# Optimization experiments

Measured on AMD Instinct MI355X. Metric: run time of the kernel, lower is better.

Reference implementation:

```python
import jax, jax.numpy as jnp
import numpy as np

S, B, E, H, V = 512, 256, 256, 256, 50000


def setup_inputs() -> dict:
    key = jax.random.key(0)
    ks = jax.random.split(key, 16)
    sc = 0.05
    return {
        "s1": jax.random.randint(ks[0], (S, B), 0, V, dtype=jnp.int32),
        "s2": jax.random.randint(ks[1], (S, B), 0, V, dtype=jnp.int32),
        "emb": jax.random.normal(ks[2], (V, E), jnp.float32) * sc,
        "W_ih": jax.random.normal(ks[3], (4 * H, E), jnp.float32) * sc,
        "W_hh": jax.random.normal(ks[4], (4 * H, H), jnp.float32) * sc,
        "b_ih": jax.random.normal(ks[5], (4 * H,), jnp.float32) * sc,
        "b_hh": jax.random.normal(ks[6], (4 * H,), jnp.float32) * sc,
        "h0_1": jax.random.normal(ks[7], (B, H), jnp.float32),
        "c0_1": jax.random.normal(ks[8], (B, H), jnp.float32),
        "h0_2": jax.random.normal(ks[9], (B, H), jnp.float32),
        "c0_2": jax.random.normal(ks[10], (B, H), jnp.float32),
        "W1": jax.random.normal(ks[11], (H, 2 * H), jnp.float32) * sc,
        "b1": jax.random.normal(ks[12], (H,), jnp.float32) * sc,
        "W2": jax.random.normal(ks[13], (2, H), jnp.float32) * sc,
        "b2": jax.random.normal(ks[14], (2,), jnp.float32) * sc,
    }


def _lstm(tokens, emb, W_ih, W_hh, b_ih, b_hh, h0, c0):
    # tokens: [S, B] int; returns final hidden h: [B, H]
    x = emb[tokens]  # [S, B, E]
    b = b_ih + b_hh

    def step(carry, xt):
        h, c = carry
        gates = xt @ W_ih.T + h @ W_hh.T + b  # [B, 4H]
        i, f, g, o = jnp.split(gates, 4, axis=-1)  # PyTorch gate order
        i = jax.nn.sigmoid(i)
        f = jax.nn.sigmoid(f)
        g = jnp.tanh(g)
        o = jax.nn.sigmoid(o)
        c = f * c + i * g
        h = o * jnp.tanh(c)
        return (h, c), None

    (h, c), _ = jax.lax.scan(step, (h0, c0), x)
    return h


def reference(s1, s2, emb, W_ih, W_hh, b_ih, b_hh, h0_1, c0_1, h0_2, c0_2, W1, b1, W2, b2):
    v1 = _lstm(s1, emb, W_ih, W_hh, b_ih, b_hh, h0_1, c0_1)  # [B, H]
    v2 = _lstm(s2, emb, W_ih, W_hh, b_ih, b_hh, h0_2, c0_2)  # [B, H]
    feat = jnp.concatenate([v1, v2], axis=-1)  # [B, 2H]
    hid = feat @ W1.T + b1  # no activation, per original Sequential
    out = hid @ W2.T + b2  # [B, 2]
    return out
```

## Files before the change

### kernel.cpp

```cpp
#include <hip/hip_runtime.h>
#include <hip/hip_bf16.h>

#define SS 512
#define BB 256
#define EE 256
#define HH 256
#define VV 50000
#define NCH 512
#define VR 16

#define NGRP 32
#define NSLC 8

#define CTRL_CNT 0
#define CTRL_START 32
#define CTRL_UNSAFE 33
#define CTRL_CLAIMG 34
#define CTRL_CLAIMX 40
#define CTRL_FLAGS 64
#define CTRL_N (64 + NGRP * NSLC * 16)

__device__ __forceinline__ float sigf(float x) { return 1.f / (1.f + __expf(-x)); }
__device__ __forceinline__ float tanhf_fast(float x) { return 1.f - 2.f / (__expf(2.f * x) + 1.f); }

__global__ void pack_w4(const float* __restrict__ W, float4* __restrict__ Wp, int K) {
    int idx = blockIdx.x * blockDim.x + threadIdx.x;
    if (idx >= K * HH) return;
    int k = idx >> 8, t = idx & 255;
    Wp[idx] = make_float4(W[(0 * HH + t) * K + k], W[(1 * HH + t) * K + k],
                          W[(2 * HH + t) * K + k], W[(3 * HH + t) * K + k]);
}

__global__ void pack_b(const float* __restrict__ bi, const float* __restrict__ bh,
                       float4* __restrict__ bp) {
    int t = threadIdx.x;
    bp[t] = make_float4(bi[0 * HH + t] + bh[0 * HH + t], bi[1 * HH + t] + bh[1 * HH + t],
                        bi[2 * HH + t] + bh[2 * HH + t], bi[3 * HH + t] + bh[3 * HH + t]);
}

__global__ void transpose_w1(const float* __restrict__ W1, float* __restrict__ W1T) {
    int idx = blockIdx.x * blockDim.x + threadIdx.x;
    if (idx >= 2 * HH * HH) return;
    int k = idx >> 8, j = idx & 255;
    W1T[idx] = W1[j * (2 * HH) + k];
}

__global__ void zero_ctrl(int* __restrict__ p) {
    int i = blockIdx.x * blockDim.x + threadIdx.x;
    if (i < CTRL_N) p[i] = 0;
}

__global__ __launch_bounds__(256) void embw_kernel(const float* __restrict__ emb,
                                                   const float4* __restrict__ Wip,
                                                   const float4* __restrict__ bp,
                                                   float4* __restrict__ embWp) {
    __shared__ float se[VR][EE];
    int t = threadIdx.x;
    int v0 = blockIdx.x * VR;
    for (int r = 0; r < VR; ++r) se[r][t] = emb[(size_t)(v0 + r) * EE + t];
    __syncthreads();
    float4 bb = bp[t];
    float4 acc[VR];
#pragma unroll
    for (int r = 0; r < VR; ++r) acc[r] = bb;
#pragma unroll 2
    for (int k = 0; k < EE; ++k) {
        float4 w = Wip[k * HH + t];
#pragma unroll
        for (int r = 0; r < VR; ++r) {
            float x = se[r][k];
            acc[r].x += w.x * x; acc[r].y += w.y * x;
            acc[r].z += w.z * x; acc[r].w += w.w * x;
        }
    }
    for (int r = 0; r < VR; ++r) embWp[(size_t)(v0 + r) * HH + t] = acc[r];
}

__global__ __launch_bounds__(256, 1) void lstm_coop(
    const int* __restrict__ s1, const int* __restrict__ s2,
    const float4* __restrict__ Whp, const float4* __restrict__ embWp,
    const float* __restrict__ h0_1, const float* __restrict__ c0_1,
    const float* __restrict__ h0_2, const float* __restrict__ c0_2,
    float* __restrict__ feat, float* __restrict__ hbuf, int* __restrict__ ctrl) {
    __shared__ float4 w4s[256 * 32];
    __shared__ float4 hls4[256 * 4];
    __shared__ int shi[4];

    const int t = threadIdx.x;
    const int j = t & 31, ks = (t >> 5) & 1, mg = t >> 6;

    if (t == 0) {
        int my_xcd = (int)__builtin_amdgcn_s_getreg(63508) & 7;
        int slot = atomicAdd(&ctrl[CTRL_CLAIMX + my_xcd], 1);
        int wall = atomicAdd(&ctrl[CTRL_CLAIMG], 1);
        if (slot >= 32)
            __hip_atomic_fetch_or(&ctrl[CTRL_UNSAFE], 1, __ATOMIC_RELAXED,
                                  __HIP_MEMORY_SCOPE_AGENT);
        __hip_atomic_fetch_add(&ctrl[CTRL_START], 1, __ATOMIC_RELEASE,
                               __HIP_MEMORY_SCOPE_AGENT);
        long it = 0;
        while (__hip_atomic_load(&ctrl[CTRL_START], __ATOMIC_ACQUIRE,
                                 __HIP_MEMORY_SCOPE_AGENT) < NGRP * NSLC) {
            if (++it >= 3000000L) break;
            __builtin_amdgcn_s_sleep(2);
        }
        int uns = __hip_atomic_load(&ctrl[CTRL_UNSAFE], __ATOMIC_ACQUIRE,
                                    __HIP_MEMORY_SCOPE_AGENT);
        if (uns) { shi[0] = wall >> 3; shi[1] = wall & 7; }
        else     { shi[0] = my_xcd * 4 + (slot >> 3); shi[1] = slot & 7; }
        shi[2] = uns;
    }
    __syncthreads();
    const int gid = shi[0];
    const int u = shi[1];
    const bool safe = (shi[2] == 0);
    const int u32j = u * 32 + j;

    for (int idx = t; idx < 256 * 32; idx += 256)
        w4s[idx] = Whp[(idx >> 5) * HH + u * 32 + (idx & 31)];

    const bool tw2 = gid >= 16;
    const float* h0x = tw2 ? h0_2 : h0_1;
    const float* c0x = tw2 ? c0_2 : c0_1;
    const int* tp = tw2 ? s2 : s1;
    const int gb = (gid & 15) * 16;

    float* hptr = (float*)hls4;
#pragma unroll
    for (int q = 0; q < 16; ++q) {
        int e = t + q * 256;
        hptr[e] = h0x[(gb + (e & 15)) * HH + (e >> 4)];
    }
    float c[4];
#pragma unroll
    for (int i = 0; i < 4; ++i) c[i] = c0x[(gb + mg * 4 + i) * HH + u32j];
    __syncthreads();

    const int bq0 = gb + mg * 4 + 2 * ks;
    float4 pfv[2]; int tnx[2];
    {
        int tk0 = tp[0 * BB + bq0], tk1 = tp[0 * BB + bq0 + 1];
        pfv[0] = embWp[(size_t)tk0 * HH + u32j];
        pfv[1] = embWp[(size_t)tk1 * HH + u32j];
        tnx[0] = tp[1 * BB + bq0];
        tnx[1] = tp[1 * BB + bq0 + 1];
    }

    const float4* wp = w4s + ks * 128 * 32 + j;
    const float4* hp = hls4 + ks * 128 * 4 + mg;
    volatile int* fl = (volatile int*)(ctrl + CTRL_FLAGS + gid * NSLC * 16);
    int dead = 0;

    for (int s = 0; s < SS; ++s) {
        float4 pf2[2]; int t2[2];
        pf2[0] = embWp[(size_t)tnx[0] * HH + u32j];
        pf2[1] = embWp[(size_t)tnx[1] * HH + u32j];
        int sn = (s + 2 < SS) ? s + 2 : SS - 1;
        t2[0] = tp[sn * BB + bq0];
        t2[1] = tp[sn * BB + bq0 + 1];

        float4 a0 = {0, 0, 0, 0}, a1 = {0, 0, 0, 0}, a2 = {0, 0, 0, 0}, a3 = {0, 0, 0, 0};
#pragma unroll 4
        for (int kk = 0; kk < 128; ++kk) {
            float4 w = wp[kk * 32];
            float4 h4 = hp[kk * 4];
            a0.x += w.x * h4.x; a0.y += w.y * h4.x; a0.z += w.z * h4.x; a0.w += w.w * h4.x;
            a1.x += w.x * h4.y; a1.y += w.y * h4.y; a1.z += w.z * h4.y; a1.w += w.w * h4.y;
            a2.x += w.x * h4.z; a2.y += w.y * h4.z; a2.z += w.z * h4.z; a2.w += w.w * h4.z;
            a3.x += w.x * h4.w; a3.y += w.y * h4.w; a3.z += w.z * h4.w; a3.w += w.w * h4.w;
        }
        if (ks == 0) {
            a0.x += pfv[0].x; a0.y += pfv[0].y; a0.z += pfv[0].z; a0.w += pfv[0].w;
            a1.x += pfv[1].x; a1.y += pfv[1].y; a1.z += pfv[1].z; a1.w += pfv[1].w;
        } else {
            a2.x += pfv[0].x; a2.y += pfv[0].y; a2.z += pfv[0].z; a2.w += pfv[0].w;
            a3.x += pfv[1].x; a3.y += pfv[1].y; a3.z += pfv[1].z; a3.w += pfv[1].w;
        }
        a0.x += __shfl_xor(a0.x, 32); a0.y += __shfl_xor(a0.y, 32);
        a0.z += __shfl_xor(a0.z, 32); a0.w += __shfl_xor(a0.w, 32);
        a1.x += __shfl_xor(a1.x, 32); a1.y += __shfl_xor(a1.y, 32);
        a1.z += __shfl_xor(a1.z, 32); a1.w += __shfl_xor(a1.w, 32);
        a2.x += __shfl_xor(a2.x, 32); a2.y += __shfl_xor(a2.y, 32);
        a2.z += __shfl_xor(a2.z, 32); a2.w += __shfl_xor(a2.w, 32);
        a3.x += __shfl_xor(a3.x, 32); a3.y += __shfl_xor(a3.y, 32);
        a3.z += __shfl_xor(a3.z, 32); a3.w += __shfl_xor(a3.w, 32);

        float hn[4];
        {
            float ig, fg, gg, og;
            ig = sigf(a0.x); fg = sigf(a0.y); gg = tanhf_fast(a0.z); og = sigf(a0.w);
            c[0] = fg * c[0] + ig * gg; hn[0] = og * tanhf_fast(c[0]);
            ig = sigf(a1.x); fg = sigf(a1.y); gg = tanhf_fast(a1.z); og = sigf(a1.w);
            c[1] = fg * c[1] + ig * gg; hn[1] = og * tanhf_fast(c[1]);
            ig = sigf(a2.x); fg = sigf(a2.y); gg = tanhf_fast(a2.z); og = sigf(a2.w);
            c[2] = fg * c[2] + ig * gg; hn[2] = og * tanhf_fast(c[2]);
            ig = sigf(a3.x); fg = sigf(a3.y); gg = tanhf_fast(a3.z); og = sigf(a3.w);
            c[3] = fg * c[3] + ig * gg; hn[3] = og * tanhf_fast(c[3]);
        }
        float* hx = hbuf + ((s + 1) & 1) * (NGRP * 16 * HH) + gid * (16 * HH);
        if (ks == 0) {
            *((float4*)(hx + u32j * 16 + mg * 4)) =
                make_float4(hn[0], hn[1], hn[2], hn[3]);
        }
        __syncthreads();
        if (safe) {
            if (t == 0) {
                fl[u * 16] = s + 1;
                if (!dead) {
                    long it = 0;
                    for (;;) {
                        int ok = 1;
#pragma unroll
                        for (int x = 0; x < NSLC; ++x) ok &= (fl[x * 16] >= s + 1);
                        if (ok) break;
                        if (++it >= 400000L) { dead = 1; break; }
                    }
                }
            }
        } else {
            __threadfence();
            if (t == 0) {
                atomicAdd(&ctrl[CTRL_CNT + gid], 1);
                int tgt = NSLC * (s + 1);
                if (!dead) {
                    long it = 0;
                    while (__hip_atomic_load(&ctrl[CTRL_CNT + gid], __ATOMIC_RELAXED,
                                             __HIP_MEMORY_SCOPE_AGENT) < tgt) {
                        if (++it >= 4000000L) { dead = 1; break; }
                        __builtin_amdgcn_s_sleep(2);
                    }
                }
            }
        }
        __syncthreads();
        if (!safe) __threadfence();
        const volatile float* hsrc = (const volatile float*)hx;
#pragma unroll
        for (int q = 0; q < 16; ++q) {
            int e = t + q * 256;
            hptr[e] = hsrc[e];
        }
        __syncthreads();
        pfv[0] = pf2[0]; pfv[1] = pf2[1];
        tnx[0] = t2[0]; tnx[1] = t2[1];
    }

    if (u == 0) {
#pragma unroll
        for (int q = 0; q < 16; ++q) {
            int e = t + q * 256;
            feat[(size_t)(gid * 16 + (e & 15)) * HH + (e >> 4)] = hptr[e];
        }
    }
}

#define NBF 4
__global__ __launch_bounds__(256, 1) void lstm_stream(
    const int* __restrict__ s1, const int* __restrict__ s2, const float* __restrict__ emb,
    const float4* __restrict__ Whp, const float4* __restrict__ Wip,
    const float4* __restrict__ bp,
    const float* __restrict__ h0_1, const float* __restrict__ c0_1,
    const float* __restrict__ h0_2, const float* __restrict__ c0_2,
    float* __restrict__ feat) {
    __shared__ float hs[NBF][HH];
    __shared__ float xs[NBF][EE];
    int t = threadIdx.x;
    int ch0 = blockIdx.x * NBF;
    float c[NBF];
    int bat[NBF];
    const int* toks[NBF];
#pragma unroll
    for (int nb = 0; nb < NBF; ++nb) {
        int ch = ch0 + nb;
        bool t2 = ch >= BB;
        int b = t2 ? ch - BB : ch;
        bat[nb] = b;
        toks[nb] = t2 ? s2 : s1;
        hs[nb][t] = (t2 ? h0_2 : h0_1)[b * HH + t];
        c[nb] = (t2 ? c0_2 : c0_1)[b * HH + t];
    }
    __syncthreads();
    for (int s = 0; s < SS; ++s) {
        float4 acc[NBF];
        float4 bb = bp[t];
#pragma unroll
        for (int nb = 0; nb < NBF; ++nb) {
            int tok = toks[nb][s * BB + bat[nb]];
            xs[nb][t] = emb[(size_t)tok * EE + t];
            acc[nb] = bb;
        }
        __syncthreads();
#pragma unroll 4
        for (int k = 0; k < EE; ++k) {
            float4 w = Wip[k * HH + t];
#pragma unroll
            for (int nb = 0; nb < NBF; ++nb) {
                float x = xs[nb][k];
                acc[nb].x += w.x * x; acc[nb].y += w.y * x;
                acc[nb].z += w.z * x; acc[nb].w += w.w * x;
            }
        }
#pragma unroll 8
        for (int k = 0; k < HH; ++k) {
            float4 w = Whp[k * HH + t];
#pragma unroll
            for (int nb = 0; nb < NBF; ++nb) {
                float hk = hs[nb][k];
                acc[nb].x += w.x * hk; acc[nb].y += w.y * hk;
                acc[nb].z += w.z * hk; acc[nb].w += w.w * hk;
            }
        }
        float hnew[NBF];
#pragma unroll
        for (int nb = 0; nb < NBF; ++nb) {
            float ig = sigf(acc[nb].x), fg = sigf(acc[nb].y);
            float gg = tanhf_fast(acc[nb].z), og = sigf(acc[nb].w);
            c[nb] = fg * c[nb] + ig * gg;
            hnew[nb] = og * tanhf_fast(c[nb]);
        }
        __syncthreads();
#pragma unroll
        for (int nb = 0; nb < NBF; ++nb) hs[nb][t] = hnew[nb];
        __syncthreads();
    }
#pragma unroll
    for (int nb = 0; nb < NBF; ++nb) feat[(size_t)(ch0 + nb) * HH + t] = hs[nb][t];
}

__global__ __launch_bounds__(256) void head_kernel(const float* __restrict__ feat,
                                                   const float* __restrict__ W1T,
                                                   const float* __restrict__ b1,
                                                   const float* __restrict__ W2,
                                                   const float* __restrict__ b2,
                                                   float* __restrict__ out) {
    __shared__ float f[2 * HH];
    __shared__ float r0[256], r1[256];
    int j = threadIdx.x;
    int b = blockIdx.x;
    f[j] = feat[(size_t)b * HH + j];
    f[HH + j] = feat[(size_t)(BB + b) * HH + j];
    __syncthreads();
    float acc = b1[j];
#pragma unroll 4
    for (int k = 0; k < 2 * HH; ++k) acc += f[k] * W1T[k * HH + j];
    r0[j] = acc * W2[0 * HH + j];
    r1[j] = acc * W2[1 * HH + j];
    __syncthreads();
    for (int st = 128; st > 0; st >>= 1) {
        if (j < st) { r0[j] += r0[j + st]; r1[j] += r1[j + st]; }
        __syncthreads();
    }
    if (j == 0) {
        out[b * 2 + 0] = r0[0] + b2[0];
        out[b * 2 + 1] = r1[0] + b2[1];
    }
}

extern "C" void kernel_launch(void* const* d_in, const int* in_sizes, int n_in,
                              void* d_out, int out_size, void* d_ws, size_t ws_size,
                              hipStream_t stream) {
    const int* s1 = (const int*)d_in[0];
    const int* s2 = (const int*)d_in[1];
    const float* emb = (const float*)d_in[2];
    const float* W_ih = (const float*)d_in[3];
    const float* W_hh = (const float*)d_in[4];
    const float* b_ih = (const float*)d_in[5];
    const float* b_hh = (const float*)d_in[6];
    const float* h0_1 = (const float*)d_in[7];
    const float* c0_1 = (const float*)d_in[8];
    const float* h0_2 = (const float*)d_in[9];
    const float* c0_2 = (const float*)d_in[10];
    const float* W1 = (const float*)d_in[11];
    const float* b1 = (const float*)d_in[12];
    const float* W2 = (const float*)d_in[13];
    const float* b2 = (const float*)d_in[14];
    float* out = (float*)d_out;

    char* ws = (char*)d_ws;
    size_t off = 0;
    auto alloc = [&](size_t bytes) {
        void* p = ws + off;
        off += (bytes + 255) & ~(size_t)255;
        return p;
    };
    float4* Whp = (float4*)alloc((size_t)HH * HH * sizeof(float4));
    float4* Wip = (float4*)alloc((size_t)EE * HH * sizeof(float4));
    float4* bp = (float4*)alloc(HH * sizeof(float4));
    float* W1T = (float*)alloc((size_t)2 * HH * HH * sizeof(float));
    float* feat = (float*)alloc((size_t)NCH * HH * sizeof(float));
    float* hbuf = (float*)alloc((size_t)2 * NGRP * 16 * HH * sizeof(float));
    int* ctrl = (int*)alloc(CTRL_N * sizeof(int));
    size_t embw_bytes = (size_t)VV * HH * sizeof(float4);
    bool pre = (ws_size >= off + embw_bytes);
    float4* embWp = pre ? (float4*)alloc(embw_bytes) : nullptr;

    pack_w4<<<(HH * HH + 255) / 256, 256, 0, stream>>>(W_ih, Wip, EE);
    pack_w4<<<(HH * HH + 255) / 256, 256, 0, stream>>>(W_hh, Whp, HH);
    pack_b<<<1, 256, 0, stream>>>(b_ih, b_hh, bp);
    transpose_w1<<<(2 * HH * HH + 255) / 256, 256, 0, stream>>>(W1, W1T);

    if (pre) {
        zero_ctrl<<<(CTRL_N + 255) / 256, 256, 0, stream>>>(ctrl);
        embw_kernel<<<VV / VR, 256, 0, stream>>>(emb, Wip, bp, embWp);
        lstm_coop<<<NGRP * NSLC, 256, 0, stream>>>(s1, s2, Whp, embWp,
                                                   h0_1, c0_1, h0_2, c0_2,
                                                   feat, hbuf, ctrl);
    } else {
        lstm_stream<<<NCH / NBF, 256, 0, stream>>>(s1, s2, emb, Whp, Wip, bp,
                                                   h0_1, c0_1, h0_2, c0_2, feat);
    }
    head_kernel<<<BB, 256, 0, stream>>>(feat, W1T, b1, W2, b2, out);
}
```

Measured before the change: 5.476 ms.

## Keep recurrent weights in registers and split K across lanes with shuffle reduction

The recurrent weight slice now lives in 32 float4 registers per thread instead of shared memory. Each thread handles one output column over a 32-wide K chunk for all 16 batch rows, and a three-level butterfly shuffle reduction combines the eight K chunks. The hidden-state exchange buffer is also laid out in padded 20-float blocks to avoid LDS bank conflicts. This removes the per-step weight reads from shared memory, but raises register pressure (128 VGPRs for weights plus 64 accumulators) and adds shuffle work.

```diff
diff --git a/kernel.cpp b/kernel.cpp
--- a/kernel.cpp
+++ b/kernel.cpp
@@ -11,6 +11,7 @@
 
 #define NGRP 32
 #define NSLC 8
+#define HWRD (256 * 20)
 
 #define CTRL_CNT 0
 #define CTRL_START 32
@@ -82,12 +83,12 @@
     const float* __restrict__ h0_1, const float* __restrict__ c0_1,
     const float* __restrict__ h0_2, const float* __restrict__ c0_2,
     float* __restrict__ feat, float* __restrict__ hbuf, int* __restrict__ ctrl) {
-    __shared__ float4 w4s[256 * 32];
-    __shared__ float4 hls4[256 * 4];
+    __shared__ float hls[16384 + HWRD];
     __shared__ int shi[4];
 
     const int t = threadIdx.x;
-    const int j = t & 31, ks = (t >> 5) & 1, mg = t >> 6;
+    const int w = t >> 6, l = t & 63;
+    const int kq = l >> 3, jl = l & 7;
 
     if (t == 0) {
         int my_xcd = (int)__builtin_amdgcn_s_getreg(63508) & 7;
@@ -114,10 +115,12 @@
     const int gid = shi[0];
     const int u = shi[1];
     const bool safe = (shi[2] == 0);
-    const int u32j = u * 32 + j;
-
-    for (int idx = t; idx < 256 * 32; idx += 256)
-        w4s[idx] = Whp[(idx >> 5) * HH + u * 32 + (idx & 31)];
+    const int gu = u * 32 + w * 8 + jl;
+
+    float4 wreg[32];
+#pragma unroll
+    for (int kk = 0; kk < 32; ++kk)
+        wreg[kk] = Whp[(kq * 32 + kk) * HH + gu];
 
     const bool tw2 = gid >= 16;
     const float* h0x = tw2 ? h0_2 : h0_1;
@@ -125,83 +128,106 @@
     const int* tp = tw2 ? s2 : s1;
     const int gb = (gid & 15) * 16;
 
-    float* hptr = (float*)hls4;
-#pragma unroll
-    for (int q = 0; q < 16; ++q) {
-        int e = t + q * 256;
-        hptr[e] = h0x[(gb + (e & 15)) * HH + (e >> 4)];
-    }
-    float c[4];
-#pragma unroll
-    for (int i = 0; i < 4; ++i) c[i] = c0x[(gb + mg * 4 + i) * HH + u32j];
-    __syncthreads();
-
-    const int bq0 = gb + mg * 4 + 2 * ks;
+    for (int e = t; e < HWRD; e += 256) {
+        int blk = e / 20, cc = e % 20;
+        int k = (blk & 7) * 32 + (blk >> 3);
+        hls[e] = (cc < 16) ? h0x[(gb + cc) * HH + k] : 0.f;
+    }
+    float cst[2];
+    cst[0] = c0x[(gb + 2 * kq + 0) * HH + gu];
+    cst[1] = c0x[(gb + 2 * kq + 1) * HH + gu];
+    __syncthreads();
+
+    const int bq0 = gb + 2 * kq;
     float4 pfv[2]; int tnx[2];
-    {
-        int tk0 = tp[0 * BB + bq0], tk1 = tp[0 * BB + bq0 + 1];
-        pfv[0] = embWp[(size_t)tk0 * HH + u32j];
-        pfv[1] = embWp[(size_t)tk1 * HH + u32j];
-        tnx[0] = tp[1 * BB + bq0];
-        tnx[1] = tp[1 * BB + bq0 + 1];
-    }
-
-    const float4* wp = w4s + ks * 128 * 32 + j;
-    const float4* hp = hls4 + ks * 128 * 4 + mg;
+    pfv[0] = embWp[(size_t)tp[bq0] * HH + gu];
+    pfv[1] = embWp[(size_t)tp[bq0 + 1] * HH + gu];
+    tnx[0] = tp[BB + bq0];
+    tnx[1] = tp[BB + bq0 + 1];
+
+    const float4* hl4 = (const float4*)hls;
     volatile int* fl = (volatile int*)(ctrl + CTRL_FLAGS + gid * NSLC * 16);
+    const int b0 = kq & 1, b1 = (kq >> 1) & 1, b2 = kq >> 2;
+    const int blkd = ((gu & 31) * 8 + (gu >> 5)) * 20 + 2 * kq;
     int dead = 0;
 
     for (int s = 0; s < SS; ++s) {
         float4 pf2[2]; int t2[2];
-        pf2[0] = embWp[(size_t)tnx[0] * HH + u32j];
-        pf2[1] = embWp[(size_t)tnx[1] * HH + u32j];
+        pf2[0] = embWp[(size_t)tnx[0] * HH + gu];
+        pf2[1] = embWp[(size_t)tnx[1] * HH + gu];
         int sn = (s + 2 < SS) ? s + 2 : SS - 1;
         t2[0] = tp[sn * BB + bq0];
         t2[1] = tp[sn * BB + bq0 + 1];
 
-        float4 a0 = {0, 0, 0, 0}, a1 = {0, 0, 0, 0}, a2 = {0, 0, 0, 0}, a3 = {0, 0, 0, 0};
-#pragma unroll 4
-        for (int kk = 0; kk < 128; ++kk) {
-            float4 w = wp[kk * 32];
-            float4 h4 = hp[kk * 4];
-            a0.x += w.x * h4.x; a0.y += w.y * h4.x; a0.z += w.z * h4.x; a0.w += w.w * h4.x;
-            a1.x += w.x * h4.y; a1.y += w.y * h4.y; a1.z += w.z * h4.y; a1.w += w.w * h4.y;
-            a2.x += w.x * h4.z; a2.y += w.y * h4.z; a2.z += w.z * h4.z; a2.w += w.w * h4.z;
-            a3.x += w.x * h4.w; a3.y += w.y * h4.w; a3.z += w.z * h4.w; a3.w += w.w * h4.w;
-        }
-        if (ks == 0) {
-            a0.x += pfv[0].x; a0.y += pfv[0].y; a0.z += pfv[0].z; a0.w += pfv[0].w;
-            a1.x += pfv[1].x; a1.y += pfv[1].y; a1.z += pfv[1].z; a1.w += pfv[1].w;
-        } else {
-            a2.x += pfv[0].x; a2.y += pfv[0].y; a2.z += pfv[0].z; a2.w += pfv[0].w;
-            a3.x += pfv[1].x; a3.y += pfv[1].y; a3.z += pfv[1].z; a3.w += pfv[1].w;
-        }
-        a0.x += __shfl_xor(a0.x, 32); a0.y += __shfl_xor(a0.y, 32);
-        a0.z += __shfl_xor(a0.z, 32); a0.w += __shfl_xor(a0.w, 32);
-        a1.x += __shfl_xor(a1.x, 32); a1.y += __shfl_xor(a1.y, 32);
-        a1.z += __shfl_xor(a1.z, 32); a1.w += __shfl_xor(a1.w, 32);
-        a2.x += __shfl_xor(a2.x, 32); a2.y += __shfl_xor(a2.y, 32);
-        a2.z += __shfl_xor(a2.z, 32); a2.w += __shfl_xor(a2.w, 32);
-        a3.x += __shfl_xor(a3.x, 32); a3.y += __shfl_xor(a3.y, 32);
-        a3.z += __shfl_xor(a3.z, 32); a3.w += __shfl_xor(a3.w, 32);
-
-        float hn[4];
+        float4 acc[16];
+#pragma unroll
+        for (int c = 0; c < 16; ++c) acc[c] = make_float4(0.f, 0.f, 0.f, 0.f);
+#pragma unroll
+        for (int kk = 0; kk < 32; ++kk) {
+            const float4 wv = wreg[kk];
+            const int base = (kk * 8 + kq) * 5;
+            const float4 hv0 = hl4[base + 0], hv1 = hl4[base + 1];
+            const float4 hv2 = hl4[base + 2], hv3 = hl4[base + 3];
+#define FMA4(C, HV) acc[C].x += wv.x * HV; acc[C].y += wv.y * HV; \
+                    acc[C].z += wv.z * HV; acc[C].w += wv.w * HV;
+            FMA4(0, hv0.x) FMA4(1, hv0.y) FMA4(2, hv0.z) FMA4(3, hv0.w)
+            FMA4(4, hv1.x) FMA4(5, hv1.y) FMA4(6, hv1.z) FMA4(7, hv1.w)
+            FMA4(8, hv2.x) FMA4(9, hv2.y) FMA4(10, hv2.z) FMA4(11, hv2.w)
+            FMA4(12, hv3.x) FMA4(13, hv3.y) FMA4(14, hv3.z) FMA4(15, hv3.w)
+#undef FMA4
+        }
+
+        float4 s1v[8];
         {
-            float ig, fg, gg, og;
-            ig = sigf(a0.x); fg = sigf(a0.y); gg = tanhf_fast(a0.z); og = sigf(a0.w);
-            c[0] = fg * c[0] + ig * gg; hn[0] = og * tanhf_fast(c[0]);
-            ig = sigf(a1.x); fg = sigf(a1.y); gg = tanhf_fast(a1.z); og = sigf(a1.w);
-            c[1] = fg * c[1] + ig * gg; hn[1] = og * tanhf_fast(c[1]);
-            ig = sigf(a2.x); fg = sigf(a2.y); gg = tanhf_fast(a2.z); og = sigf(a2.w);
-            c[2] = fg * c[2] + ig * gg; hn[2] = og * tanhf_fast(c[2]);
-            ig = sigf(a3.x); fg = sigf(a3.y); gg = tanhf_fast(a3.z); og = sigf(a3.w);
-            c[3] = fg * c[3] + ig * gg; hn[3] = og * tanhf_fast(c[3]);
-        }
-        float* hx = hbuf + ((s + 1) & 1) * (NGRP * 16 * HH) + gid * (16 * HH);
-        if (ks == 0) {
-            *((float4*)(hx + u32j * 16 + mg * 4)) =
-                make_float4(hn[0], hn[1], hn[2], hn[3]);
-        }
+#pragma unroll
+            for (int i = 0; i < 8; ++i) {
+                constexpr int LO[8] = {0, 1, 4, 5, 8, 9, 12, 13};
+                float4 xs = b0 ? acc[LO[i]] : acc[LO[i] + 2];
+                float4 kp = b0 ? acc[LO[i] + 2] : acc[LO[i]];
+                s1v[i].x = kp.x + __shfl_xor(xs.x, 8);
+                s1v[i].y = kp.y + __shfl_xor(xs.y, 8);
+                s1v[i].z = kp.z + __shfl_xor(xs.z, 8);
+                s1v[i].w = kp.w + __shfl_xor(xs.w, 8);
+            }
+        }
+        float4 s2v[4];
+        {
+#pragma unroll
+            for (int i = 0; i < 4; ++i) {
+                constexpr int A2[4] = {0, 1, 4, 5};
+                float4 xs = b1 ? s1v[A2[i]] : s1v[A2[i] ^ 2];
+                float4 kp = b1 ? s1v[A2[i] ^ 2] : s1v[A2[i]];
+                s2v[i].x = kp.x + __shfl_xor(xs.x, 16);
+                s2v[i].y = kp.y + __shfl_xor(xs.y, 16);
+                s2v[i].z = kp.z + __shfl_xor(xs.z, 16);
+                s2v[i].w = kp.w + __shfl_xor(xs.w, 16);
+            }
+        }
+        float4 g2[2];
+#pragma unroll
+        for (int i = 0; i < 2; ++i) {
+            float4 xs = b2 ? s2v[i] : s2v[i + 2];
+            float4 kp = b2 ? s2v[i + 2] : s2v[i];
+            g2[i].x = kp.x + __shfl_xor(xs.x, 32);
+            g2[i].y = kp.y + __shfl_xor(xs.y, 32);
+            g2[i].z = kp.z + __shfl_xor(xs.z, 32);
+            g2[i].w = kp.w + __shfl_xor(xs.w, 32);
+        }
+
+        float hn0, hn1;
+        {
+            g2[0].x += pfv[0].x; g2[0].y += pfv[0].y; g2[0].z += pfv[0].z; g2[0].w += pfv[0].w;
+            g2[1].x += pfv[1].x; g2[1].y += pfv[1].y; g2[1].z += pfv[1].z; g2[1].w += pfv[1].w;
+            float ig = sigf(g2[0].x), fg = sigf(g2[0].y);
+            float gg = tanhf_fast(g2[0].z), og = sigf(g2[0].w);
+            cst[0] = fg * cst[0] + ig * gg; hn0 = og * tanhf_fast(cst[0]);
+            ig = sigf(g2[1].x); fg = sigf(g2[1].y);
+            gg = tanhf_fast(g2[1].z); og = sigf(g2[1].w);
+            cst[1] = fg * cst[1] + ig * gg; hn1 = og * tanhf_fast(cst[1]);
+        }
+
+        float* hx = hbuf + ((s + 1) & 1) * (NGRP * HWRD) + gid * HWRD;
+        *(float2*)(hx + blkd) = make_float2(hn0, hn1);
         __syncthreads();
         if (safe) {
             if (t == 0) {
@@ -234,22 +260,21 @@
         }
         __syncthreads();
         if (!safe) __threadfence();
-        const volatile float* hsrc = (const volatile float*)hx;
-#pragma unroll
-        for (int q = 0; q < 16; ++q) {
-            int e = t + q * 256;
-            hptr[e] = hsrc[e];
-        }
+        const volatile float* hv = (const volatile float*)hx;
+#pragma unroll
+        for (int q = 0; q < 20; ++q) hls[q * 256 + t] = hv[q * 256 + t];
         __syncthreads();
         pfv[0] = pf2[0]; pfv[1] = pf2[1];
         tnx[0] = t2[0]; tnx[1] = t2[1];
     }
 
     if (u == 0) {
-#pragma unroll
-        for (int q = 0; q < 16; ++q) {
-            int e = t + q * 256;
-            feat[(size_t)(gid * 16 + (e & 15)) * HH + (e >> 4)] = hptr[e];
+        for (int e = t; e < HWRD; e += 256) {
+            int blk = e / 20, cc = e % 20;
+            if (cc < 16) {
+                int k = (blk & 7) * 32 + (blk >> 3);
+                feat[(size_t)(gid * 16 + cc) * HH + k] = hls[e];
+            }
         }
     }
 }
@@ -388,7 +413,7 @@
     float4* bp = (float4*)alloc(HH * sizeof(float4));
     float* W1T = (float*)alloc((size_t)2 * HH * HH * sizeof(float));
     float* feat = (float*)alloc((size_t)NCH * HH * sizeof(float));
-    float* hbuf = (float*)alloc((size_t)2 * NGRP * 16 * HH * sizeof(float));
+    float* hbuf = (float*)alloc((size_t)2 * NGRP * HWRD * sizeof(float));
     int* ctrl = (int*)alloc(CTRL_N * sizeof(int));
     size_t embw_bytes = (size_t)VV * HH * sizeof(float4);
     bool pre = (ws_size >= off + embw_bytes);
```

New measurement: 12.48 ms. 128% more time.
